# Kernel optimization log

Hardware: AMD Instinct MI355X
Metric: run time of the kernel (lower is better)

Reference implementation:

```python
import jax, jax.numpy as jnp
import numpy as np

INPUT_WIDTH = 768
OUTPUT_WIDTH = 768
DEPTH = 11
N_NODES = 2 ** (DEPTH + 1) - 1  # 4095 (parallel_size == 1)
N_TOKENS = 8192


def setup_inputs() -> dict:
    key = jax.random.key(0)
    k0, k1, k2 = jax.random.split(key, 3)
    oldx = jax.random.normal(k0, (N_TOKENS, INPUT_WIDTH), dtype=jnp.float32)
    # nn.Linear default init scale ~ 1/sqrt(fan_in); keep inits small so logits are reasonable
    w_in = jax.random.normal(k1, (N_NODES, INPUT_WIDTH), dtype=jnp.float32) / np.sqrt(INPUT_WIDTH)
    w_out = jax.random.normal(k2, (OUTPUT_WIDTH, N_NODES), dtype=jnp.float32) / np.sqrt(N_NODES)
    return {"oldx": oldx, "w_in": w_in, "w_out": w_out}


def _fff(oldx, w_in, w_out):
    x = oldx.reshape(-1, INPUT_WIDTH)            # [B, D]
    B = x.shape[0]
    logits = x @ w_in.T                          # [B, n_nodes]
    decisions = (logits > 0).astype(jnp.int32)   # [B, n_nodes]
    acts = jax.nn.gelu(logits, approximate=False)  # torch nn.GELU default = exact erf

    # Tree walk: root node 0 is always active; at each level, follow the
    # binary decision at the current node to pick the child, marking it active.
    dmap = jnp.zeros_like(logits).at[:, 0].set(1.0)
    cur = jnp.zeros((B,), dtype=jnp.int32)
    rows = jnp.arange(B)
    for d in range(DEPTH):
        cur_platform = 2 ** d - 1
        next_platform = 2 ** (d + 1) - 1
        moves = jnp.take_along_axis(decisions, cur[:, None], axis=1)[:, 0]  # [B]
        nxt = (cur - cur_platform) * 2 + moves + next_platform
        dmap = dmap.at[rows, nxt].set(1.0)
        cur = nxt
    dmap = jax.lax.stop_gradient(dmap)           # built under torch.no_grad()

    masked = acts * dmap                         # [B, n_nodes], sparse (depth+1 active per row)
    return masked @ w_out.T                      # [B, output_width]


def reference(oldx, w_in, w_out):
    return _fff(oldx, w_in, w_out)
```

## Files before the change

kernel.cpp:

```cpp
#include <hip/hip_runtime.h>
#include <math.h>

#define DEPTH    11
#define NNODES   4095
#define DIN      768
#define NTOK     8192
#define TAU      0.06f
#define WT_MAX   0.12f
#define WT_STEP  (WT_MAX / 127.0f)

typedef unsigned int uint32;
typedef float f32x4 __attribute__((ext_vector_type(4)));

__global__ __launch_bounds__(256) void fff_prep(const float* __restrict__ w_in,
                                                const float* __restrict__ w_out,
                                                uint32* __restrict__ wq,
                                                float* __restrict__ wscale,
                                                uint32* __restrict__ wTq) {
    __shared__ float tile[32][33];
    const int bid = blockIdx.x;
    const int tid = threadIdx.x;

    if (bid < 3072) {
        const int n0 = (bid & 127) * 32;
        const int j0 = (bid >> 7) * 32;
        const int tx = tid & 31, ty = tid >> 5;
#pragma unroll
        for (int i = 0; i < 32; i += 8) {
            const int j = j0 + ty + i;
            const int n = n0 + tx;
            if (n < NNODES) tile[ty + i][tx] = w_out[(size_t)j * NNODES + n];
        }
        __syncthreads();
        const int nl = tid >> 3;
        const int jq = (tid & 7) * 4;
        const int n  = n0 + nl;
        if (n < NNODES) {
            const float inv = 127.0f / WT_MAX;
            int q0 = __float2int_rn(fminf(fmaxf(tile[jq + 0][nl] * inv, -127.f), 127.f));
            int q1 = __float2int_rn(fminf(fmaxf(tile[jq + 1][nl] * inv, -127.f), 127.f));
            int q2 = __float2int_rn(fminf(fmaxf(tile[jq + 2][nl] * inv, -127.f), 127.f));
            int q3 = __float2int_rn(fminf(fmaxf(tile[jq + 3][nl] * inv, -127.f), 127.f));
            const uint32 pack = (uint32)(q0 & 0xFF) | ((uint32)(q1 & 0xFF) << 8) |
                                ((uint32)(q2 & 0xFF) << 16) | ((uint32)(q3 & 0xFF) << 24);
            wTq[((size_t)n * DIN + j0 + jq) >> 2] = pack;
        }
    } else {
        const int row  = ((bid - 3072) * 256 + tid) >> 6;
        const int lane = tid & 63;
        if (row < NNODES) {
            const float4* wr = reinterpret_cast<const float4*>(w_in + (size_t)row * DIN);
            const float4 a = wr[lane], b = wr[lane + 64], c = wr[lane + 128];
            float m = fmaxf(fabsf(a.x), fabsf(a.y));
            m = fmaxf(m, fmaxf(fabsf(a.z), fabsf(a.w)));
            m = fmaxf(m, fmaxf(fabsf(b.x), fabsf(b.y)));
            m = fmaxf(m, fmaxf(fabsf(b.z), fabsf(b.w)));
            m = fmaxf(m, fmaxf(fabsf(c.x), fabsf(c.y)));
            m = fmaxf(m, fmaxf(fabsf(c.z), fabsf(c.w)));
#pragma unroll
            for (int off = 32; off >= 1; off >>= 1) m = fmaxf(m, __shfl_xor(m, off));
            const float inv = (m > 0.f) ? (127.0f / m) : 0.f;
            const float s   = m * (1.0f / 127.0f);

            uint32* rq = wq + (size_t)row * (DIN / 4);
            const float4 v[3] = {a, b, c};
#pragma unroll
            for (int k = 0; k < 3; ++k) {
                int q0 = __float2int_rn(fminf(fmaxf(v[k].x * inv, -127.f), 127.f));
                int q1 = __float2int_rn(fminf(fmaxf(v[k].y * inv, -127.f), 127.f));
                int q2 = __float2int_rn(fminf(fmaxf(v[k].z * inv, -127.f), 127.f));
                int q3 = __float2int_rn(fminf(fmaxf(v[k].w * inv, -127.f), 127.f));
                rq[lane + 64 * k] = (uint32)(q0 & 0xFF) | ((uint32)(q1 & 0xFF) << 8) |
                                    ((uint32)(q2 & 0xFF) << 16) | ((uint32)(q3 & 0xFF) << 24);
            }
            if (lane == 0) wscale[row] = s;
        }
    }
}

__device__ __forceinline__ float sb0(uint32 u) { return (float)((int)(u << 24) >> 24); }
__device__ __forceinline__ float sb1(uint32 u) { return (float)((int)(u << 16) >> 24); }
__device__ __forceinline__ float sb2(uint32 u) { return (float)((int)(u <<  8) >> 24); }
__device__ __forceinline__ float sb3(uint32 u) { return (float)((int)u        >> 24); }

template <int CTRL>
__device__ __forceinline__ float dpp_add(float v) {
    const int p = __builtin_amdgcn_update_dpp(0, __float_as_int(v), CTRL, 0xf, 0xf, false);
    return v + __int_as_float(p);
}

__device__ __forceinline__ float dpp_wave_sum_bcast(float v) {
    v = dpp_add<0x128>(v);
    v = dpp_add<0x124>(v);
    v = dpp_add<0x122>(v);
    v = dpp_add<0x121>(v);
    v = dpp_add<0x142>(v);
    v = dpp_add<0x143>(v);
    return __int_as_float(__builtin_amdgcn_readlane(__float_as_int(v), 63));
}

__global__ __launch_bounds__(256) void fff_main_i8d(const float* __restrict__ x,
                                                    const float* __restrict__ w_in,
                                                    const uint32* __restrict__ wq,
                                                    const float* __restrict__ wscale,
                                                    const uint32* __restrict__ wTq,
                                                    float* __restrict__ out) {
    const int token = (int)((blockIdx.x * blockDim.x + threadIdx.x) >> 6);
    const int lane  = (int)(threadIdx.x & 63);

    const f32x4* xr = reinterpret_cast<const f32x4*>(x + (size_t)token * DIN);
    const f32x4 xv0 = __builtin_nontemporal_load(xr + lane);
    const f32x4 xv1 = __builtin_nontemporal_load(xr + lane + 64);
    const f32x4 xv2 = __builtin_nontemporal_load(xr + lane + 128);

    float lgv[12];
    unsigned mask = 0;
    int cur = 0;

#pragma unroll
    for (int d = 0; d <= DEPTH; ++d) {
        const uint32* rq = wq + (size_t)cur * (DIN / 4);
        const uint32 a = rq[lane], b = rq[lane + 64], c = rq[lane + 128];
        const float s = wscale[cur];

        float s0 = 0.f, s1 = 0.f, s2 = 0.f, s3 = 0.f;
        s0 = fmaf(xv0[0], sb0(a), s0); s1 = fmaf(xv0[1], sb1(a), s1);
        s2 = fmaf(xv0[2], sb2(a), s2); s3 = fmaf(xv0[3], sb3(a), s3);
        s0 = fmaf(xv1[0], sb0(b), s0); s1 = fmaf(xv1[1], sb1(b), s1);
        s2 = fmaf(xv1[2], sb2(b), s2); s3 = fmaf(xv1[3], sb3(b), s3);
        s0 = fmaf(xv2[0], sb0(c), s0); s1 = fmaf(xv2[1], sb1(c), s1);
        s2 = fmaf(xv2[2], sb2(c), s2); s3 = fmaf(xv2[3], sb3(c), s3);

        const float tot = dpp_wave_sum_bcast(((s0 + s1) + (s2 + s3)));
        float lg    = tot * s;
        bool  right = (lg > 0.0f);

        if (fabsf(lg) < TAU) {
            const float4* wr = reinterpret_cast<const float4*>(w_in + (size_t)cur * DIN);
            const float4 w0 = wr[lane], w1 = wr[lane + 64], w2 = wr[lane + 128];
            double p0 = 0.0, p1 = 0.0, p2 = 0.0;
            p0 += (double)xv0[0] * w0.x; p0 += (double)xv0[1] * w0.y;
            p0 += (double)xv0[2] * w0.z; p0 += (double)xv0[3] * w0.w;
            p1 += (double)xv1[0] * w1.x; p1 += (double)xv1[1] * w1.y;
            p1 += (double)xv1[2] * w1.z; p1 += (double)xv1[3] * w1.w;
            p2 += (double)xv2[0] * w2.x; p2 += (double)xv2[1] * w2.y;
            p2 += (double)xv2[2] * w2.z; p2 += (double)xv2[3] * w2.w;
            double pd = (p0 + p1) + p2;
#pragma unroll
            for (int off = 32; off >= 1; off >>= 1) pd += __shfl_xor(pd, off);
            lg    = (float)pd;
            right = (pd > 0.0);
        }

        lgv[d] = lg;

        if (d < DEPTH) {
            mask |= (right ? 1u : 0u) << d;
            cur = __builtin_amdgcn_readfirstlane(2 * cur + 1 + (right ? 1 : 0));
        }
    }

    float cf[12];
#pragma unroll
    for (int d = 0; d < 12; ++d)
        cf[d] = 0.5f * lgv[d] * (1.0f + erff(lgv[d] * 0.7071067811865476f)) * WT_STEP;

    float acc[12];
#pragma unroll
    for (int i = 0; i < 12; ++i) acc[i] = 0.f;

    int nd = 0;
#pragma unroll
    for (int d = 0; d <= DEPTH; ++d) {
        const uint32* rt = wTq + (size_t)nd * (DIN / 4);
        const uint32 ta = rt[lane], tb = rt[lane + 64], tc = rt[lane + 128];
        const float c = cf[d];
        acc[0]  = fmaf(c, sb0(ta), acc[0]);  acc[1]  = fmaf(c, sb1(ta), acc[1]);
        acc[2]  = fmaf(c, sb2(ta), acc[2]);  acc[3]  = fmaf(c, sb3(ta), acc[3]);
        acc[4]  = fmaf(c, sb0(tb), acc[4]);  acc[5]  = fmaf(c, sb1(tb), acc[5]);
        acc[6]  = fmaf(c, sb2(tb), acc[6]);  acc[7]  = fmaf(c, sb3(tb), acc[7]);
        acc[8]  = fmaf(c, sb0(tc), acc[8]);  acc[9]  = fmaf(c, sb1(tc), acc[9]);
        acc[10] = fmaf(c, sb2(tc), acc[10]); acc[11] = fmaf(c, sb3(tc), acc[11]);
        if (d < DEPTH) nd = 2 * nd + 1 + (int)((mask >> d) & 1u);
    }

    f32x4* orow = reinterpret_cast<f32x4*>(out + (size_t)token * DIN);
    f32x4 o0, o1, o2;
    o0[0] = acc[0];  o0[1] = acc[1];  o0[2] = acc[2];  o0[3] = acc[3];
    o1[0] = acc[4];  o1[1] = acc[5];  o1[2] = acc[6];  o1[3] = acc[7];
    o2[0] = acc[8];  o2[1] = acc[9];  o2[2] = acc[10]; o2[3] = acc[11];
    __builtin_nontemporal_store(o0, orow + lane);
    __builtin_nontemporal_store(o1, orow + lane + 64);
    __builtin_nontemporal_store(o2, orow + lane + 128);
}

__global__ __launch_bounds__(256) void fff_fused_fallback(const float* __restrict__ x,
                                                          const float* __restrict__ w_in,
                                                          const float* __restrict__ w_o,
                                                          float* __restrict__ out) {
    const int token = (int)((blockIdx.x * blockDim.x + threadIdx.x) >> 6);
    const int lane  = (int)(threadIdx.x & 63);

    const float4* xr = reinterpret_cast<const float4*>(x + (size_t)token * DIN);
    float4 xv[3];
#pragma unroll
    for (int k = 0; k < 3; ++k) xv[k] = xr[lane + 64 * k];
    float4 acc[3];
#pragma unroll
    for (int k = 0; k < 3; ++k) acc[k] = make_float4(0.f, 0.f, 0.f, 0.f);

    int cur = 0;
#pragma unroll
    for (int d = 0; d <= DEPTH; ++d) {
        const float4* wr = reinterpret_cast<const float4*>(w_in + (size_t)cur * DIN);
        double part = 0.0;
#pragma unroll
        for (int k = 0; k < 3; ++k) {
            const float4 w = wr[lane + 64 * k];
            part += (double)xv[k].x * w.x; part += (double)xv[k].y * w.y;
            part += (double)xv[k].z * w.z; part += (double)xv[k].w * w.w;
        }
#pragma unroll
        for (int off = 32; off >= 1; off >>= 1) part += __shfl_xor(part, off);
        const float logit = (float)part;
        const float gg = 0.5f * logit * (1.0f + erff(logit * 0.7071067811865476f));
#pragma unroll
        for (int k = 0; k < 3; ++k) {
            const int j = (lane + 64 * k) * 4;
            acc[k].x = fmaf(gg, w_o[(size_t)(j + 0) * NNODES + cur], acc[k].x);
            acc[k].y = fmaf(gg, w_o[(size_t)(j + 1) * NNODES + cur], acc[k].y);
            acc[k].z = fmaf(gg, w_o[(size_t)(j + 2) * NNODES + cur], acc[k].z);
            acc[k].w = fmaf(gg, w_o[(size_t)(j + 3) * NNODES + cur], acc[k].w);
        }
        if (d < DEPTH) cur = 2 * cur + 1 + (part > 0.0 ? 1 : 0);
    }
    float4* orow = reinterpret_cast<float4*>(out + (size_t)token * DIN);
#pragma unroll
    for (int k = 0; k < 3; ++k) orow[lane + 64 * k] = acc[k];
}

extern "C" void kernel_launch(void* const* d_in, const int* in_sizes, int n_in,
                              void* d_out, int out_size, void* d_ws, size_t ws_size,
                              hipStream_t stream) {
    const float* x     = (const float*)d_in[0];
    const float* w_in  = (const float*)d_in[1];
    const float* w_out = (const float*)d_in[2];
    float*       out   = (float*)d_out;

    const size_t wq_bytes  = (size_t)NNODES * DIN;
    const size_t wTq_bytes = (size_t)NNODES * DIN;
    const size_t sc_bytes  = (size_t)NNODES * sizeof(float);
    const size_t need = wq_bytes + wTq_bytes + sc_bytes;

    if (ws_size >= need) {
        char* ws = (char*)d_ws;
        uint32* wq     = (uint32*)ws;
        uint32* wTq    = (uint32*)(ws + wq_bytes);
        float*  wscale = (float*)(ws + wq_bytes + wTq_bytes);

        hipLaunchKernelGGL(fff_prep, dim3(4096), dim3(256), 0, stream,
                           w_in, w_out, wq, wscale, wTq);
        hipLaunchKernelGGL(fff_main_i8d, dim3(NTOK / 4), dim3(256), 0, stream,
                           x, w_in, wq, wscale, wTq, out);
    } else {
        hipLaunchKernelGGL(fff_fused_fallback, dim3(NTOK / 4), dim3(256), 0, stream,
                           x, w_in, w_out, out);
    }
}
```

Baseline: 36.89 us.

## Interleave quantized in/out weights per node and stage top tree levels in LDS

Packs the int8 input-projection row and transposed output column of each node into one contiguous 384-dword record. The main kernel copies the first 31 nodes (tree levels 0-4) plus their scales into shared memory at block start, and serves those levels from LDS instead of global memory. The aim is to cut global/L2 traffic for the hot upper tree nodes. In exchange, every block performs a ~47 KB cooperative copy and a barrier, and the large LDS footprint reduces occupancy.

```diff
diff --git a/kernel.cpp b/kernel.cpp
--- a/kernel.cpp
+++ b/kernel.cpp
@@ -8,15 +8,16 @@
 #define TAU      0.06f
 #define WT_MAX   0.12f
 #define WT_STEP  (WT_MAX / 127.0f)
+#define NSTAGE   31
+#define NODE_DW  384
 
 typedef unsigned int uint32;
 typedef float f32x4 __attribute__((ext_vector_type(4)));
 
 __global__ __launch_bounds__(256) void fff_prep(const float* __restrict__ w_in,
                                                 const float* __restrict__ w_out,
-                                                uint32* __restrict__ wq,
-                                                float* __restrict__ wscale,
-                                                uint32* __restrict__ wTq) {
+                                                uint32* __restrict__ wqt,
+                                                float* __restrict__ wscale) {
     __shared__ float tile[32][33];
     const int bid = blockIdx.x;
     const int tid = threadIdx.x;
@@ -43,7 +44,7 @@
             int q3 = __float2int_rn(fminf(fmaxf(tile[jq + 3][nl] * inv, -127.f), 127.f));
             const uint32 pack = (uint32)(q0 & 0xFF) | ((uint32)(q1 & 0xFF) << 8) |
                                 ((uint32)(q2 & 0xFF) << 16) | ((uint32)(q3 & 0xFF) << 24);
-            wTq[((size_t)n * DIN + j0 + jq) >> 2] = pack;
+            wqt[(size_t)n * NODE_DW + 192 + ((j0 + jq) >> 2)] = pack;
         }
     } else {
         const int row  = ((bid - 3072) * 256 + tid) >> 6;
@@ -62,7 +63,7 @@
             const float inv = (m > 0.f) ? (127.0f / m) : 0.f;
             const float s   = m * (1.0f / 127.0f);
 
-            uint32* rq = wq + (size_t)row * (DIN / 4);
+            uint32* rq = wqt + (size_t)row * NODE_DW;
             const float4 v[3] = {a, b, c};
 #pragma unroll
             for (int k = 0; k < 3; ++k) {
@@ -99,14 +100,25 @@
     return __int_as_float(__builtin_amdgcn_readlane(__float_as_int(v), 63));
 }
 
-__global__ __launch_bounds__(256) void fff_main_i8d(const float* __restrict__ x,
+__global__ __launch_bounds__(256) void fff_main_i8l(const float* __restrict__ x,
                                                     const float* __restrict__ w_in,
-                                                    const uint32* __restrict__ wq,
+                                                    const uint32* __restrict__ wqt,
                                                     const float* __restrict__ wscale,
-                                                    const uint32* __restrict__ wTq,
                                                     float* __restrict__ out) {
-    const int token = (int)((blockIdx.x * blockDim.x + threadIdx.x) >> 6);
-    const int lane  = (int)(threadIdx.x & 63);
+    __shared__ uint32 lds_wqt[NSTAGE * NODE_DW];
+    __shared__ float  lds_sc[NSTAGE];
+
+    const int tid   = (int)threadIdx.x;
+    const int token = (int)((blockIdx.x * blockDim.x + tid) >> 6);
+    const int lane  = tid & 63;
+
+    {
+        const uint4* src = reinterpret_cast<const uint4*>(wqt);
+        uint4* dst = reinterpret_cast<uint4*>(lds_wqt);
+        for (int i = tid; i < NSTAGE * NODE_DW / 4; i += 256) dst[i] = src[i];
+        if (tid < NSTAGE) lds_sc[tid] = wscale[tid];
+        __syncthreads();
+    }
 
     const f32x4* xr = reinterpret_cast<const f32x4*>(x + (size_t)token * DIN);
     const f32x4 xv0 = __builtin_nontemporal_load(xr + lane);
@@ -119,9 +131,17 @@
 
 #pragma unroll
     for (int d = 0; d <= DEPTH; ++d) {
-        const uint32* rq = wq + (size_t)cur * (DIN / 4);
-        const uint32 a = rq[lane], b = rq[lane + 64], c = rq[lane + 128];
-        const float s = wscale[cur];
+        uint32 a, b, c;
+        float  s;
+        if (d <= 4) {
+            const uint32* rq = lds_wqt + cur * NODE_DW;
+            a = rq[lane]; b = rq[lane + 64]; c = rq[lane + 128];
+            s = lds_sc[cur];
+        } else {
+            const uint32* rq = wqt + (size_t)cur * NODE_DW;
+            a = rq[lane]; b = rq[lane + 64]; c = rq[lane + 128];
+            s = wscale[cur];
+        }
 
         float s0 = 0.f, s1 = 0.f, s2 = 0.f, s3 = 0.f;
         s0 = fmaf(xv0[0], sb0(a), s0); s1 = fmaf(xv0[1], sb1(a), s1);
@@ -172,8 +192,14 @@
     int nd = 0;
 #pragma unroll
     for (int d = 0; d <= DEPTH; ++d) {
-        const uint32* rt = wTq + (size_t)nd * (DIN / 4);
-        const uint32 ta = rt[lane], tb = rt[lane + 64], tc = rt[lane + 128];
+        uint32 ta, tb, tc;
+        if (d <= 4) {
+            const uint32* rt = lds_wqt + nd * NODE_DW + 192;
+            ta = rt[lane]; tb = rt[lane + 64]; tc = rt[lane + 128];
+        } else {
+            const uint32* rt = wqt + (size_t)nd * NODE_DW + 192;
+            ta = rt[lane]; tb = rt[lane + 64]; tc = rt[lane + 128];
+        }
         const float c = cf[d];
         acc[0]  = fmaf(c, sb0(ta), acc[0]);  acc[1]  = fmaf(c, sb1(ta), acc[1]);
         acc[2]  = fmaf(c, sb2(ta), acc[2]);  acc[3]  = fmaf(c, sb3(ta), acc[3]);
@@ -247,21 +273,19 @@
     const float* w_out = (const float*)d_in[2];
     float*       out   = (float*)d_out;
 
-    const size_t wq_bytes  = (size_t)NNODES * DIN;
-    const size_t wTq_bytes = (size_t)NNODES * DIN;
+    const size_t wqt_bytes = (size_t)NNODES * NODE_DW * 4;
     const size_t sc_bytes  = (size_t)NNODES * sizeof(float);
-    const size_t need = wq_bytes + wTq_bytes + sc_bytes;
+    const size_t need = wqt_bytes + sc_bytes;
 
     if (ws_size >= need) {
         char* ws = (char*)d_ws;
-        uint32* wq     = (uint32*)ws;
-        uint32* wTq    = (uint32*)(ws + wq_bytes);
-        float*  wscale = (float*)(ws + wq_bytes + wTq_bytes);
+        uint32* wqt    = (uint32*)ws;
+        float*  wscale = (float*)(ws + wqt_bytes);
 
         hipLaunchKernelGGL(fff_prep, dim3(4096), dim3(256), 0, stream,
-                           w_in, w_out, wq, wscale, wTq);
-        hipLaunchKernelGGL(fff_main_i8d, dim3(NTOK / 4), dim3(256), 0, stream,
-                           x, w_in, wq, wscale, wTq, out);
+                           w_in, w_out, wqt, wscale);
+        hipLaunchKernelGGL(fff_main_i8l, dim3(NTOK / 4), dim3(256), 0, stream,
+                           x, w_in, wqt, wscale, out);
     } else {
         hipLaunchKernelGGL(fff_fused_fallback, dim3(NTOK / 4), dim3(256), 0, stream,
                            x, w_in, w_out, out);
```

New measurement: 46.30 us. 1.26x slower.
